# Kernel tuning notes

Measured on AMD Instinct MI355X. Metric: run time of the kernel, lower is better.

## Reference

```python
import jax, jax.numpy as jnp
import numpy as np

N = 2048


def setup_inputs() -> dict:
    key = jax.random.key(0)
    k1, k2 = jax.random.split(key)
    graph1 = jax.random.uniform(k1, (N, N), dtype=jnp.float32)
    graph2 = jax.random.uniform(k2, (N, N), dtype=jnp.float32)
    return {"graph1": graph1, "graph2": graph2}


def _degree_dist(adj):
    return adj.sum(axis=-1)


def _clustering(adj):
    # diag(A @ A @ A) computed without materializing the full cube:
    # tri_i = sum_j (A@A)_{ij} * A_{ji}
    a2 = adj @ adj                      # [n, n]
    tri = (a2 * adj.T).sum(axis=-1)     # [n]
    deg = adj.sum(axis=-1)
    deg = jnp.where(deg < 2, 1.0, deg)  # torch: deg[deg < 2] = 1
    return tri / (deg * (deg - 1.0))


def reference(graph1, graph2):
    d1 = _degree_dist(graph1)
    d2 = _degree_dist(graph2)
    degree_sim = jnp.exp(-jnp.abs(d1 - d2).mean())
    c1 = _clustering(graph1)
    c2 = _clustering(graph2)
    cluster_sim = jnp.exp(-jnp.abs(c1 - c2).mean())
    overall = (degree_sim + cluster_sim) / 2.0
    return (degree_sim, cluster_sim, overall)
```

## Files before the change

### kernel.cpp

```cpp
#include <hip/hip_runtime.h>

#define NN 2048

typedef unsigned short u16;
typedef __attribute__((ext_vector_type(8))) short short8;
typedef __attribute__((ext_vector_type(4))) float floatx4;

__device__ __forceinline__ u16 f2bf(float f) {
  unsigned u = __float_as_uint(f);
  u += 0x7FFF + ((u >> 16) & 1);
  return (u16)(u >> 16);
}

__device__ __forceinline__ float bf2f(u16 h) {
  return __uint_as_float(((unsigned)h) << 16);
}

__device__ __forceinline__ void load_lds16(const u16* g, u16* l) {
  __builtin_amdgcn_global_load_lds(
      (const __attribute__((address_space(1))) unsigned int*)g,
      (__attribute__((address_space(3))) unsigned int*)l,
      16, 0, 0);
}

__global__ __launch_bounds__(256) void prep_kernel(
    const float* __restrict__ A1, const float* __restrict__ A2,
    u16* __restrict__ Abf, u16* __restrict__ AbfT,
    float* __restrict__ degp, float* __restrict__ tri) {
  __shared__ u16 Tl[64][68];
  const int bx = blockIdx.x, by = blockIdx.y, bz = blockIdx.z;
  const float* __restrict__ A = bz ? A2 : A1;
  u16* __restrict__ ab = Abf + (size_t)bz * (NN * (size_t)NN);
  u16* __restrict__ at = AbfT + (size_t)bz * (NN * (size_t)NN);
  float* __restrict__ dp = degp + (size_t)bz * (32 * NN);
  const int t = threadIdx.x;
  const int r0 = by * 64, c0 = bx * 64;
  const int rs = t >> 4, cs = t & 15;

  if (bx == 0 && t < 64) tri[bz * NN + by * 64 + t] = 0.f;

#pragma unroll
  for (int it = 0; it < 4; ++it) {
    const int r = it * 16 + rs;
    const float4 fv = *(const float4*)(A + (size_t)(r0 + r) * NN + c0 + cs * 4);
    ushort4 b;
    b.x = f2bf(fv.x); b.y = f2bf(fv.y); b.z = f2bf(fv.z); b.w = f2bf(fv.w);
    *(ushort4*)(ab + (size_t)(r0 + r) * NN + c0 + cs * 4) = b;
    Tl[r][cs * 4 + 0] = b.x; Tl[r][cs * 4 + 1] = b.y;
    Tl[r][cs * 4 + 2] = b.z; Tl[r][cs * 4 + 3] = b.w;
    float s = fv.x + fv.y + fv.z + fv.w;
    s += __shfl_xor(s, 1); s += __shfl_xor(s, 2);
    s += __shfl_xor(s, 4); s += __shfl_xor(s, 8);
    if (cs == 0) dp[(r0 + r) * 32 + bx] = s;
  }
  __syncthreads();
#pragma unroll
  for (int it = 0; it < 4; ++it) {
    const int c = it * 16 + rs;
    ushort4 b;
    b.x = Tl[cs * 4 + 0][c]; b.y = Tl[cs * 4 + 1][c];
    b.z = Tl[cs * 4 + 2][c]; b.w = Tl[cs * 4 + 3][c];
    *(ushort4*)(at + (size_t)(c0 + c) * NN + r0 + cs * 4) = b;
  }
}

__global__ __launch_bounds__(256) void gemm_tri_kernel(
    const u16* __restrict__ Abf, const u16* __restrict__ AbfT,
    float* __restrict__ tri) {
  __shared__ u16 smem[17408];

  const int tid = threadIdx.x;
  const int w = tid >> 6, lane = tid & 63;
  const int wm = w >> 1, wn = w & 1;
  const int cl = lane & 15, g = lane >> 4;
  const int i0 = blockIdx.y * 128, j0 = blockIdx.x * 128;
  const size_t mat = (size_t)blockIdx.z * (NN * (size_t)NN);
  const u16* __restrict__ Am = Abf + mat;
  const u16* __restrict__ ATm = AbfT + mat;
  float* __restrict__ triM = tri + blockIdx.z * NN;

  const int s0 = (w * 2 + 0) * 64 + lane;
  const int s1 = (w * 2 + 1) * 64 + lane;
  const int r0s = s0 >> 2, c0s = (s0 & 3) ^ ((r0s >> 1) & 3);
  const int r1s = s1 >> 2, c1s = (s1 & 3) ^ ((r1s >> 1) & 3);
  const u16* gA0 = Am + (size_t)(i0 + r0s) * NN + c0s * 8;
  const u16* gA1 = Am + (size_t)(i0 + r1s) * NN + c1s * 8;
  const u16* gB0 = ATm + (size_t)(j0 + r0s) * NN + c0s * 8;
  const u16* gB1 = ATm + (size_t)(j0 + r1s) * NN + c1s * 8;
  const int sA0 = (w * 2 + 0) * 512, sA1 = (w * 2 + 1) * 512;
  const int sB0 = 4096 + sA0, sB1 = 4096 + sA1;

  const int swz = g ^ ((cl >> 1) & 3);
  int aoff[4], boff[4];
#pragma unroll
  for (int tm = 0; tm < 4; ++tm)
    aoff[tm] = (wm * 64 + tm * 16 + cl) * 32 + swz * 8;
#pragma unroll
  for (int tn = 0; tn < 4; ++tn)
    boff[tn] = 4096 + (wn * 64 + tn * 16 + cl) * 32 + swz * 8;

  floatx4 acc[4][4] = {};

  {
    u16* base = smem;
    load_lds16(gA0, base + sA0);
    load_lds16(gA1, base + sA1);
    load_lds16(gB0, base + sB0);
    load_lds16(gB1, base + sB1);
  }

  for (int it = 0; it < 64; ++it) {
    const int p = it & 1;
    asm volatile("" ::: "memory");
    __builtin_amdgcn_s_barrier();
    asm volatile("" ::: "memory");
    if (it < 63) {
      const int kk = (it + 1) * 32;
      u16* base = smem + (p ^ 1) * 8192;
      load_lds16(gA0 + kk, base + sA0);
      load_lds16(gA1 + kk, base + sA1);
      load_lds16(gB0 + kk, base + sB0);
      load_lds16(gB1 + kk, base + sB1);
      __builtin_amdgcn_s_waitcnt(0x0F74);
    } else {
      __builtin_amdgcn_s_waitcnt(0x0F70);
    }
    asm volatile("" ::: "memory");
    __builtin_amdgcn_s_barrier();
    asm volatile("" ::: "memory");

    const int pb = p * 8192;
    short8 af[4], bfr[4];
#pragma unroll
    for (int tm = 0; tm < 4; ++tm)
      af[tm] = *(const short8*)(smem + pb + aoff[tm]);
#pragma unroll
    for (int tn = 0; tn < 4; ++tn)
      bfr[tn] = *(const short8*)(smem + pb + boff[tn]);
#pragma unroll
    for (int tm = 0; tm < 4; ++tm)
#pragma unroll
      for (int tn = 0; tn < 4; ++tn)
        acc[tm][tn] = __builtin_amdgcn_mfma_f32_16x16x32_bf16(
            af[tm], bfr[tn], acc[tm][tn], 0, 0, 0);
  }

  __syncthreads();
#pragma unroll
  for (int it = 0; it < 8; ++it) {
    const int idx = tid + it * 256;
    const int r = idx >> 4, co = (idx & 15) * 8;
    *(uint4*)(smem + r * 136 + co) =
        *(const uint4*)(ATm + (size_t)(i0 + r) * NN + j0 + co);
  }
  __syncthreads();

#pragma unroll
  for (int tm = 0; tm < 4; ++tm) {
#pragma unroll
    for (int reg = 0; reg < 4; ++reg) {
      const int rloc = wm * 64 + tm * 16 + g * 4 + reg;
      float v = 0.f;
#pragma unroll
      for (int tn = 0; tn < 4; ++tn) {
        const int cloc = wn * 64 + tn * 16 + cl;
        v += acc[tm][tn][reg] * bf2f(smem[rloc * 136 + cloc]);
      }
      v += __shfl_xor(v, 1);
      v += __shfl_xor(v, 2);
      v += __shfl_xor(v, 4);
      v += __shfl_xor(v, 8);
      if (cl == 0) atomicAdd(&triM[i0 + rloc], v);
    }
  }
}

__global__ __launch_bounds__(1024) void finalize1_kernel(
    const float* __restrict__ degp, const float* __restrict__ tri,
    float* __restrict__ part) {
  __shared__ float red[32];
  const int t = threadIdx.x;
  const int r = blockIdx.x * 128 + (t >> 3);
  const int q = (t & 7) * 4;
  const float4 v1 = *(const float4*)(degp + (size_t)r * 32 + q);
  const float4 v2 = *(const float4*)(degp + 32 * NN + (size_t)r * 32 + q);
  float d1 = v1.x + v1.y + v1.z + v1.w;
  float d2 = v2.x + v2.y + v2.z + v2.w;
#pragma unroll
  for (int m = 1; m < 8; m <<= 1) {
    d1 += __shfl_xor(d1, m);
    d2 += __shfl_xor(d2, m);
  }
  float sdd = 0.f, scc = 0.f;
  if ((t & 7) == 0) {
    const float t1 = tri[r], t2 = tri[NN + r];
    const float e1 = d1 < 2.f ? 1.f : d1;
    const float e2 = d2 < 2.f ? 1.f : d2;
    sdd = fabsf(d1 - d2);
    scc = fabsf(t1 / (e1 * (e1 - 1.f)) - t2 / (e2 * (e2 - 1.f)));
  }
#pragma unroll
  for (int m = 8; m < 64; m <<= 1) {
    sdd += __shfl_xor(sdd, m);
    scc += __shfl_xor(scc, m);
  }
  const int wv = t >> 6, ln = t & 63;
  if (ln == 0) { red[wv] = sdd; red[16 + wv] = scc; }
  __syncthreads();
  if (t == 0) {
    float a = 0.f, b = 0.f;
#pragma unroll
    for (int i = 0; i < 16; ++i) { a += red[i]; b += red[16 + i]; }
    part[blockIdx.x * 2 + 0] = a;
    part[blockIdx.x * 2 + 1] = b;
  }
}

__global__ void finalize2_kernel(const float* __restrict__ part,
                                 float* __restrict__ out) {
  if (threadIdx.x == 0) {
    float a = 0.f, b = 0.f;
#pragma unroll
    for (int i = 0; i < 16; ++i) { a += part[i * 2]; b += part[i * 2 + 1]; }
    const float ds = expf(-a * (1.f / (float)NN));
    const float cs = expf(-b * (1.f / (float)NN));
    out[0] = ds;
    out[1] = cs;
    out[2] = 0.5f * (ds + cs);
  }
}

extern "C" void kernel_launch(void* const* d_in, const int* in_sizes, int n_in,
                              void* d_out, int out_size, void* d_ws, size_t ws_size,
                              hipStream_t stream) {
  (void)in_sizes; (void)n_in; (void)out_size; (void)ws_size;
  const float* A1 = (const float*)d_in[0];
  const float* A2 = (const float*)d_in[1];
  float* out = (float*)d_out;

  u16* Abf = (u16*)d_ws;
  u16* AbfT = Abf + 2 * (size_t)NN * NN;
  float* tri = (float*)(AbfT + 2 * (size_t)NN * NN);
  float* degp = tri + 2 * NN;
  float* part = degp + 2 * 32 * NN;

  prep_kernel<<<dim3(32, 32, 2), 256, 0, stream>>>(A1, A2, Abf, AbfT, degp, tri);
  gemm_tri_kernel<<<dim3(16, 16, 2), 256, 0, stream>>>(Abf, AbfT, tri);
  finalize1_kernel<<<16, 1024, 0, stream>>>(degp, tri, part);
  finalize2_kernel<<<1, 64, 0, stream>>>(part, out);
}
```

Baseline: 128.0 us.

## Split GEMM K across two blocks, unroll double-buffer loop, vectorize transpose stores

The GEMM splits the K dimension in two, so the grid doubles to 1024 blocks, and partial triangle sums combine through the existing atomics. This fills the GPU's compute units better than the old 512-block grid. The main loop is unrolled by two with constant LDS buffer offsets, and launch bounds now request 4 blocks per CU. The prep transpose uses a swizzled padded LDS layout so each thread can write 16-byte vectorized rows of A^T. In exchange, each block now does a 128x128 epilogue for only half of K, and the number of atomic adds doubles.

```diff
diff --git a/kernel.cpp b/kernel.cpp
--- a/kernel.cpp
+++ b/kernel.cpp
@@ -27,7 +27,7 @@
     const float* __restrict__ A1, const float* __restrict__ A2,
     u16* __restrict__ Abf, u16* __restrict__ AbfT,
     float* __restrict__ degp, float* __restrict__ tri) {
-  __shared__ u16 Tl[64][68];
+  __shared__ u16 Tl[64 * 72];
   const int bx = blockIdx.x, by = blockIdx.y, bz = blockIdx.z;
   const float* __restrict__ A = bz ? A2 : A1;
   u16* __restrict__ ab = Abf + (size_t)bz * (NN * (size_t)NN);
@@ -36,6 +36,7 @@
   const int t = threadIdx.x;
   const int r0 = by * 64, c0 = bx * 64;
   const int rs = t >> 4, cs = t & 15;
+  const int cswz = (cs & 3) ^ (cs >> 2);
 
   if (bx == 0 && t < 64) tri[bz * NN + by * 64 + t] = 0.f;
 
@@ -46,8 +47,11 @@
     ushort4 b;
     b.x = f2bf(fv.x); b.y = f2bf(fv.y); b.z = f2bf(fv.z); b.w = f2bf(fv.w);
     *(ushort4*)(ab + (size_t)(r0 + r) * NN + c0 + cs * 4) = b;
-    Tl[r][cs * 4 + 0] = b.x; Tl[r][cs * 4 + 1] = b.y;
-    Tl[r][cs * 4 + 2] = b.z; Tl[r][cs * 4 + 3] = b.w;
+    const int chk = (it ^ cswz) * 16 + rs;
+    Tl[(cs * 4 + 0) * 72 + chk] = b.x;
+    Tl[(cs * 4 + 1) * 72 + chk] = b.y;
+    Tl[(cs * 4 + 2) * 72 + chk] = b.z;
+    Tl[(cs * 4 + 3) * 72 + chk] = b.w;
     float s = fv.x + fv.y + fv.z + fv.w;
     s += __shfl_xor(s, 1); s += __shfl_xor(s, 2);
     s += __shfl_xor(s, 4); s += __shfl_xor(s, 8);
@@ -55,16 +59,42 @@
   }
   __syncthreads();
 #pragma unroll
-  for (int it = 0; it < 4; ++it) {
-    const int c = it * 16 + rs;
-    ushort4 b;
-    b.x = Tl[cs * 4 + 0][c]; b.y = Tl[cs * 4 + 1][c];
-    b.z = Tl[cs * 4 + 2][c]; b.w = Tl[cs * 4 + 3][c];
-    *(ushort4*)(at + (size_t)(c0 + c) * NN + r0 + cs * 4) = b;
-  }
-}
-
-__global__ __launch_bounds__(256) void gemm_tri_kernel(
+  for (int p = 0; p < 2; ++p) {
+    const int cp = p * 32 + (t >> 3);
+    const int k8 = t & 7;
+    const int chunk = k8 >> 1, half = k8 & 1;
+    const int sw = chunk ^ ((cp >> 2) & 3) ^ ((cp >> 4) & 3);
+    const short8 v = *(const short8*)(Tl + cp * 72 + sw * 16 + half * 8);
+    *(short8*)(at + (size_t)(c0 + cp) * NN + r0 + k8 * 8) = v;
+  }
+}
+
+#define MFMA_BODY(PB)                                                     \
+  {                                                                       \
+    short8 af[4], bfr[4];                                                 \
+    _Pragma("unroll")                                                     \
+    for (int tm = 0; tm < 4; ++tm)                                        \
+      af[tm] = *(const short8*)(smem + (PB) + aoff[tm]);                  \
+    _Pragma("unroll")                                                     \
+    for (int tn = 0; tn < 4; ++tn)                                        \
+      bfr[tn] = *(const short8*)(smem + (PB) + boff[tn]);                 \
+    _Pragma("unroll")                                                     \
+    for (int tm = 0; tm < 4; ++tm)                                        \
+      _Pragma("unroll")                                                   \
+      for (int tn = 0; tn < 4; ++tn)                                      \
+        acc[tm][tn] = __builtin_amdgcn_mfma_f32_16x16x32_bf16(            \
+            af[tm], bfr[tn], acc[tm][tn], 0, 0, 0);                       \
+  }
+
+#define PREFETCH(KK, DB)                                                  \
+  load_lds16(gA0 + (KK), smem + (DB) + sA0);                              \
+  load_lds16(gA1 + (KK), smem + (DB) + sA1);                              \
+  load_lds16(gB0 + (KK), smem + (DB) + sB0);                              \
+  load_lds16(gB1 + (KK), smem + (DB) + sB1);
+
+#define FENCE asm volatile("" ::: "memory")
+
+__global__ __launch_bounds__(256, 4) void gemm_tri_kernel(
     const u16* __restrict__ Abf, const u16* __restrict__ AbfT,
     float* __restrict__ tri) {
   __shared__ u16 smem[17408];
@@ -74,19 +104,21 @@
   const int wm = w >> 1, wn = w & 1;
   const int cl = lane & 15, g = lane >> 4;
   const int i0 = blockIdx.y * 128, j0 = blockIdx.x * 128;
-  const size_t mat = (size_t)blockIdx.z * (NN * (size_t)NN);
+  const int mz = blockIdx.z >> 1, kz = blockIdx.z & 1;
+  const size_t mat = (size_t)mz * (NN * (size_t)NN);
   const u16* __restrict__ Am = Abf + mat;
   const u16* __restrict__ ATm = AbfT + mat;
-  float* __restrict__ triM = tri + blockIdx.z * NN;
+  float* __restrict__ triM = tri + mz * NN;
 
   const int s0 = (w * 2 + 0) * 64 + lane;
   const int s1 = (w * 2 + 1) * 64 + lane;
   const int r0s = s0 >> 2, c0s = (s0 & 3) ^ ((r0s >> 1) & 3);
   const int r1s = s1 >> 2, c1s = (s1 & 3) ^ ((r1s >> 1) & 3);
-  const u16* gA0 = Am + (size_t)(i0 + r0s) * NN + c0s * 8;
-  const u16* gA1 = Am + (size_t)(i0 + r1s) * NN + c1s * 8;
-  const u16* gB0 = ATm + (size_t)(j0 + r0s) * NN + c0s * 8;
-  const u16* gB1 = ATm + (size_t)(j0 + r1s) * NN + c1s * 8;
+  const int kbase = kz * 1024;
+  const u16* gA0 = Am + (size_t)(i0 + r0s) * NN + kbase + c0s * 8;
+  const u16* gA1 = Am + (size_t)(i0 + r1s) * NN + kbase + c1s * 8;
+  const u16* gB0 = ATm + (size_t)(j0 + r0s) * NN + kbase + c0s * 8;
+  const u16* gB1 = ATm + (size_t)(j0 + r1s) * NN + kbase + c1s * 8;
   const int sA0 = (w * 2 + 0) * 512, sA1 = (w * 2 + 1) * 512;
   const int sB0 = 4096 + sA0, sB1 = 4096 + sA1;
 
@@ -101,49 +133,30 @@
 
   floatx4 acc[4][4] = {};
 
-  {
-    u16* base = smem;
-    load_lds16(gA0, base + sA0);
-    load_lds16(gA1, base + sA1);
-    load_lds16(gB0, base + sB0);
-    load_lds16(gB1, base + sB1);
-  }
-
-  for (int it = 0; it < 64; ++it) {
-    const int p = it & 1;
-    asm volatile("" ::: "memory");
-    __builtin_amdgcn_s_barrier();
-    asm volatile("" ::: "memory");
-    if (it < 63) {
-      const int kk = (it + 1) * 32;
-      u16* base = smem + (p ^ 1) * 8192;
-      load_lds16(gA0 + kk, base + sA0);
-      load_lds16(gA1 + kk, base + sA1);
-      load_lds16(gB0 + kk, base + sB0);
-      load_lds16(gB1 + kk, base + sB1);
-      __builtin_amdgcn_s_waitcnt(0x0F74);
-    } else {
-      __builtin_amdgcn_s_waitcnt(0x0F70);
-    }
-    asm volatile("" ::: "memory");
-    __builtin_amdgcn_s_barrier();
-    asm volatile("" ::: "memory");
-
-    const int pb = p * 8192;
-    short8 af[4], bfr[4];
-#pragma unroll
-    for (int tm = 0; tm < 4; ++tm)
-      af[tm] = *(const short8*)(smem + pb + aoff[tm]);
-#pragma unroll
-    for (int tn = 0; tn < 4; ++tn)
-      bfr[tn] = *(const short8*)(smem + pb + boff[tn]);
-#pragma unroll
-    for (int tm = 0; tm < 4; ++tm)
-#pragma unroll
-      for (int tn = 0; tn < 4; ++tn)
-        acc[tm][tn] = __builtin_amdgcn_mfma_f32_16x16x32_bf16(
-            af[tm], bfr[tn], acc[tm][tn], 0, 0, 0);
-  }
+  PREFETCH(0, 0)
+
+#pragma unroll 1
+  for (int d = 0; d < 15; ++d) {
+    FENCE; __builtin_amdgcn_s_barrier(); FENCE;
+    PREFETCH((2 * d + 1) * 32, 8192)
+    __builtin_amdgcn_s_waitcnt(0x0F74);
+    FENCE; __builtin_amdgcn_s_barrier(); FENCE;
+    MFMA_BODY(0)
+    FENCE; __builtin_amdgcn_s_barrier(); FENCE;
+    PREFETCH((2 * d + 2) * 32, 0)
+    __builtin_amdgcn_s_waitcnt(0x0F74);
+    FENCE; __builtin_amdgcn_s_barrier(); FENCE;
+    MFMA_BODY(8192)
+  }
+  FENCE; __builtin_amdgcn_s_barrier(); FENCE;
+  PREFETCH(31 * 32, 8192)
+  __builtin_amdgcn_s_waitcnt(0x0F74);
+  FENCE; __builtin_amdgcn_s_barrier(); FENCE;
+  MFMA_BODY(0)
+  FENCE; __builtin_amdgcn_s_barrier(); FENCE;
+  __builtin_amdgcn_s_waitcnt(0x0F70);
+  FENCE; __builtin_amdgcn_s_barrier(); FENCE;
+  MFMA_BODY(8192)
 
   __syncthreads();
 #pragma unroll
@@ -245,7 +258,7 @@
   float* part = degp + 2 * 32 * NN;
 
   prep_kernel<<<dim3(32, 32, 2), 256, 0, stream>>>(A1, A2, Abf, AbfT, degp, tri);
-  gemm_tri_kernel<<<dim3(16, 16, 2), 256, 0, stream>>>(Abf, AbfT, tri);
+  gemm_tri_kernel<<<dim3(16, 16, 4), 256, 0, stream>>>(Abf, AbfT, tri);
   finalize1_kernel<<<16, 1024, 0, stream>>>(degp, tri, part);
   finalize2_kernel<<<1, 64, 0, stream>>>(part, out);
 }
```

After: 128.2 us. No clear change (+0.2%).
